# Performance work log

Hardware: AMD Instinct MI355X
Metric: run time of the kernel (lower is better)

Reference implementation:

```python
import jax, jax.numpy as jnp
import numpy as np

N, E, D, R = 50000, 800000, 64, 65


def setup_inputs() -> dict:
    key = jax.random.key(0)
    ks = jax.random.split(key, 8)
    x = jax.random.normal(ks[0], (N, D), dtype=jnp.float32)
    src = jax.random.randint(ks[1], (E,), 0, N, dtype=jnp.int32)
    dst = jax.random.randint(ks[2], (E,), 0, N, dtype=jnp.int32)
    edge_type = jax.random.randint(ks[3], (E,), 0, R, dtype=jnp.int32)
    s = 1.0 / np.sqrt(D)
    W1 = jax.random.normal(ks[4], (R, D, D), dtype=jnp.float32) * s
    Wl1 = jax.random.normal(ks[5], (D, D), dtype=jnp.float32) * s
    W2 = jax.random.normal(ks[6], (R, D, D), dtype=jnp.float32) * s
    Wl2 = jax.random.normal(ks[7], (D, D), dtype=jnp.float32) * s
    return {"x": x, "src": src, "dst": dst, "edge_type": edge_type,
            "W1": W1, "Wl1": Wl1, "W2": W2, "Wl2": Wl2}


def _rgcn_layer(x, src, dst, edge_type, W, Wl):
    # x: [N, D_in], W: [R, D_in, D_out], Wl: [D_in, D_out]
    n = x.shape[0]
    r = W.shape[0]
    # per-relation transform of all node features: [R, N, D_out]
    xw = jnp.einsum('nd,rdh->rnh', x, W)
    # gather transformed source feature for each edge by its relation: [E, D_out]
    msg = xw[edge_type, src]
    # mean aggregation per (destination node, relation) as in PyG RGCNConv
    key = dst.astype(jnp.int32) * r + edge_type
    cnt = jax.ops.segment_sum(jnp.ones(key.shape, x.dtype), key, num_segments=n * r)
    norm = 1.0 / jnp.maximum(cnt[key], 1.0)  # [E]
    agg = jax.ops.segment_sum(msg * norm[:, None], dst, num_segments=n)  # [N, D_out]
    # self-loop linear term (self_loop_weights in original module)
    out = agg + x @ Wl
    # activation; dropout is identity in eval mode; batch norm disabled
    return jax.nn.relu(out)


def reference(x, src, dst, edge_type, W1, Wl1, W2, Wl2):
    h = _rgcn_layer(x, src, dst, edge_type, W1, Wl1)
    h = _rgcn_layer(h, src, dst, edge_type, W2, Wl2)
    return h
```

## Files before the change

kernel.cpp:

```cpp
#include <hip/hip_runtime.h>

typedef __attribute__((ext_vector_type(8))) short bf16x8;
typedef __attribute__((ext_vector_type(4))) float f32x4;
typedef __attribute__((ext_vector_type(2))) unsigned int u32x2;

constexpr int D = 64;
constexpr int SEG = 64;
constexpr int CSTR = 16;

__device__ inline unsigned short f2bf(float f) {
  unsigned u = __float_as_uint(f);
  u += 0x7fff + ((u >> 16) & 1);
  return (unsigned short)(u >> 16);
}
__device__ inline float bflo(unsigned u) { return __uint_as_float(u << 16); }
__device__ inline float bfhi(unsigned u) { return __uint_as_float(u & 0xffff0000u); }

__global__ __launch_bounds__(256) void count_kernel(
    const int* __restrict__ dst, const int* __restrict__ et,
    int* __restrict__ bcnt, int* __restrict__ deg, int E, int R, int nbE) {
  __shared__ int lh[128];
  int t = threadIdx.x;
  if (t < 128) lh[t] = 0;
  __syncthreads();
  int e = blockIdx.x * 256 + t;
  if (e < E) {
    atomicAdd(&deg[(long)dst[e] * CSTR], 1);
    atomicAdd(&lh[et[e]], 1);
  }
  __syncthreads();
  if (t < R) bcnt[t * nbE + blockIdx.x] = lh[t];
}

__global__ __launch_bounds__(256) void scanA_dual_kernel(
    const int* __restrict__ bcnt, const int* __restrict__ deg,
    int* __restrict__ bsum, int nBC, int N, int nbBC) {
  __shared__ int s[256];
  int t = threadIdx.x;
  int b = blockIdx.x;
  int v;
  if (b < nbBC) {
    int i = b * 256 + t;
    v = (i < nBC) ? bcnt[i] : 0;
  } else {
    int i = (b - nbBC) * 256 + t;
    v = (i < N) ? deg[(long)i * CSTR] : 0;
  }
  s[t] = v;
  __syncthreads();
  for (int o = 128; o > 0; o >>= 1) {
    if (t < o) s[t] += s[t + o];
    __syncthreads();
  }
  if (t == 0) bsum[b] = s[0];
}

__device__ inline void scanB_region(int* bsum, int nb, int t) {
  __shared__ int s[256];
  __shared__ int carry;
  if (t == 0) carry = 0;
  __syncthreads();
  for (int base = 0; base < nb; base += 256) {
    int i = base + t;
    int v = (i < nb) ? bsum[i] : 0;
    s[t] = v;
    __syncthreads();
    for (int o = 1; o < 256; o <<= 1) {
      int u = (t >= o) ? s[t - o] : 0;
      __syncthreads();
      s[t] += u;
      __syncthreads();
    }
    if (i < nb) bsum[i] = carry + s[t] - v;
    __syncthreads();
    if (t == 0) carry += s[255];
    __syncthreads();
  }
}

__global__ __launch_bounds__(256) void scanB_dual_kernel(
    int* __restrict__ bsum, int nbBC, int nbN) {
  int t = threadIdx.x;
  scanB_region(bsum, nbBC, t);
  scanB_region(bsum + nbBC, nbN, t);
}

__global__ __launch_bounds__(256) void scanC_dual_kernel(
    const int* __restrict__ bcnt, const int* __restrict__ deg,
    const int* __restrict__ bsum, int* __restrict__ prefE,
    int* __restrict__ dstoff, int* __restrict__ cur2,
    int nBC, int N, int nbBC) {
  __shared__ int s[256];
  int t = threadIdx.x;
  int b = blockIdx.x;
  bool isBC = (b < nbBC);
  int i = (isBC ? b : b - nbBC) * 256 + t;
  int n = isBC ? nBC : N;
  int v = 0;
  if (i < n) v = isBC ? bcnt[i] : deg[(long)i * CSTR];
  s[t] = v;
  __syncthreads();
  for (int o = 1; o < 256; o <<= 1) {
    int u = (t >= o) ? s[t - o] : 0;
    __syncthreads();
    s[t] += u;
    __syncthreads();
  }
  int excl = bsum[b] + s[t] - v;
  if (isBC) {
    if (i < n) prefE[i] = excl;
    if (i == n - 1) prefE[n] = excl + v;
  } else {
    if (i < n) { dstoff[i] = excl; cur2[(long)i * CSTR] = excl; }
    if (i == n - 1) dstoff[n] = excl + v;
  }
}

__global__ void prefix_wrel_kernel(const int* __restrict__ prefE,
                                   int* __restrict__ cursor, int* __restrict__ wrel,
                                   int nbE, int R) {
  __shared__ int sc[128];
  int l = threadIdx.x;
  int c = 0;
  if (l < R) {
    int tot = prefE[(l + 1) * nbE] - prefE[l * nbE];
    c = (tot + SEG - 1) & ~(SEG - 1);
  }
  sc[l] = c;
  __syncthreads();
  for (int ofs = 1; ofs < 128; ofs <<= 1) {
    int v = (l >= ofs) ? sc[l - ofs] : 0;
    __syncthreads();
    sc[l] += v;
    __syncthreads();
  }
  if (l < R) {
    int cur = sc[l] - c;
    cursor[l] = cur;
    int w0 = cur >> 6;
    int nw = c >> 6;
    for (int w = 0; w < nw; ++w) wrel[w0 + w] = l;
  }
}

__global__ __launch_bounds__(256) void scatter_kernel(
    const int* __restrict__ src, const int* __restrict__ dst, const int* __restrict__ et,
    const int* __restrict__ cursor, const int* __restrict__ prefE,
    int* __restrict__ cur2, int2* __restrict__ eidx,
    int E, int R, int nbE) {
  __shared__ int lh[128];
  __shared__ int lbase[128];
  int t = threadIdx.x, b = blockIdx.x;
  if (t < R) {
    lh[t] = 0;
    lbase[t] = cursor[t] + prefE[t * nbE + b] - prefE[t * nbE];
  }
  __syncthreads();
  int e = b * 256 + t;
  if (e < E) {
    int r = et[e], s = src[e], d = dst[e];
    int lr = atomicAdd(&lh[r], 1);
    int jd = atomicAdd(&cur2[(long)d * CSTR], 1);
    int pos = lbase[r] + lr;
    eidx[pos] = make_int2(s, jd);
  }
}

__global__ __launch_bounds__(256) void cvt_all_kernel(
    const float* __restrict__ x, unsigned short* __restrict__ xb, int nx,
    const float* __restrict__ W1, unsigned short* __restrict__ WT1,
    const float* __restrict__ W2, unsigned short* __restrict__ WT2, int nw,
    const float* __restrict__ Wl1, unsigned short* __restrict__ WTl1,
    const float* __restrict__ Wl2, unsigned short* __restrict__ WTl2, int nl) {
  int i = blockIdx.x * 256 + threadIdx.x;
  if (i < nx) { xb[i] = f2bf(x[i]); return; }
  i -= nx;
  if (i < 2 * nw) {
    const float* W = (i < nw) ? W1 : W2;
    unsigned short* WT = (i < nw) ? WT1 : WT2;
    int i2 = (i < nw) ? i : i - nw;
    int n = i2 & 63, k = (i2 >> 6) & 63, r = i2 >> 12;
    WT[(r << 12) + (n << 6) + k] = f2bf(W[(r << 12) + (k << 6) + n]);
    return;
  }
  i -= 2 * nw;
  if (i < 2 * nl) {
    const float* W = (i < nl) ? Wl1 : Wl2;
    unsigned short* WT = (i < nl) ? WTl1 : WTl2;
    int i2 = (i < nl) ? i : i - nl;
    int n = i2 & 63, k = (i2 >> 6) & 63;
    WT[(n << 6) + k] = f2bf(W[(k << 6) + n]);
  }
}

__global__ __launch_bounds__(256)
void msg_kernel(const unsigned short* __restrict__ xb,
                const unsigned short* __restrict__ WT,
                const int2* __restrict__ eidx, const int* __restrict__ wrel,
                unsigned int* __restrict__ msgp, int* __restrict__ relrow, int nwaves) {
  const int lane = (int)threadIdx.x & 63;
  const int l15 = lane & 15;
  const int q = lane >> 4;
  const int wave = blockIdx.x * 4 + ((int)threadIdx.x >> 6);
  if (wave >= nwaves) return;
  const long base = (long)wave * SEG;
  const int r = wrel[wave];
  const unsigned short* wb = WT + ((long)r << 12);
  bf16x8 Bf[4][2];
#pragma unroll
  for (int nt = 0; nt < 4; ++nt)
#pragma unroll
    for (int kh = 0; kh < 2; ++kh)
      Bf[nt][kh] = *(const bf16x8*)(wb + (nt * 16 + l15) * 64 + kh * 32 + q * 8);
#pragma unroll
  for (int t = 0; t < 4; ++t) {
    int2 rec = eidx[base + t * 16 + l15];
    if (relrow && lane < 16 && rec.y >= 0) relrow[rec.y] = r;
    const unsigned short* xr = xb + ((long)max(rec.x, 0) << 6);
    bf16x8 A0 = *(const bf16x8*)(xr + q * 8);
    bf16x8 A1 = *(const bf16x8*)(xr + 32 + q * 8);
    f32x4 acc0 = (f32x4)0.0f, acc1 = (f32x4)0.0f, acc2 = (f32x4)0.0f, acc3 = (f32x4)0.0f;
    acc0 = __builtin_amdgcn_mfma_f32_16x16x32_bf16(A0, Bf[0][0], acc0, 0, 0, 0);
    acc0 = __builtin_amdgcn_mfma_f32_16x16x32_bf16(A1, Bf[0][1], acc0, 0, 0, 0);
    acc1 = __builtin_amdgcn_mfma_f32_16x16x32_bf16(A0, Bf[1][0], acc1, 0, 0, 0);
    acc1 = __builtin_amdgcn_mfma_f32_16x16x32_bf16(A1, Bf[1][1], acc1, 0, 0, 0);
    acc2 = __builtin_amdgcn_mfma_f32_16x16x32_bf16(A0, Bf[2][0], acc2, 0, 0, 0);
    acc2 = __builtin_amdgcn_mfma_f32_16x16x32_bf16(A1, Bf[2][1], acc2, 0, 0, 0);
    acc3 = __builtin_amdgcn_mfma_f32_16x16x32_bf16(A0, Bf[3][0], acc3, 0, 0, 0);
    acc3 = __builtin_amdgcn_mfma_f32_16x16x32_bf16(A1, Bf[3][1], acc3, 0, 0, 0);
#pragma unroll
    for (int rg = 0; rg < 4; ++rg) {
      int row = q * 4 + rg;
      int jd = __shfl(rec.y, row);
      if (jd >= 0) {
        unsigned p0 = (unsigned)f2bf(acc0[rg]) | ((unsigned)f2bf(acc1[rg]) << 16);
        unsigned p1 = (unsigned)f2bf(acc2[rg]) | ((unsigned)f2bf(acc3[rg]) << 16);
        u32x2 pk;
        pk.x = p0; pk.y = p1;
        *(u32x2*)(msgp + (long)jd * 32 + 2 * l15) = pk;
      }
    }
  }
}

__global__ __launch_bounds__(256) void weight_kernel(
    const int* __restrict__ relrow, const int* __restrict__ dstoff,
    float* __restrict__ wrow, int N) {
  __shared__ int rsh[4][256];
  const int wv = (int)threadIdx.x >> 6;
  const int lane = (int)threadIdx.x & 63;
  const int d = blockIdx.x * 4 + wv;
  if (d >= N) return;
  const int off = dstoff[d], end = dstoff[d + 1];
  const int deg = end - off;
  if (deg <= 0) return;
  if (deg <= 256) {
    const int nit = (deg + 63) >> 6;
    for (int it = 0; it < nit; ++it) {
      int l = it * 64 + lane;
      if (l < deg) rsh[wv][l] = relrow[off + l];
    }
    __threadfence_block();
    for (int it = 0; it < nit; ++it) {
      int l = it * 64 + lane;
      if (l < deg) {
        int rv = rsh[wv][l];
        int c = 0;
        for (int m = 0; m < deg; ++m) c += (rsh[wv][m] == rv) ? 1 : 0;
        wrow[off + l] = 1.0f / (float)c;
      }
    }
  } else {
    for (int l = lane; l < deg; l += 64) {
      int rv = relrow[off + l];
      int c = 0;
      for (int m = off; m < end; ++m) c += (relrow[m] == rv) ? 1 : 0;
      wrow[off + l] = 1.0f / (float)c;
    }
  }
}

__global__ __launch_bounds__(256) void agg_kernel(
    const unsigned int* __restrict__ msgp, const int* __restrict__ dstoff,
    const float* __restrict__ wrow, float* __restrict__ agg, int N) {
  const int lane = (int)threadIdx.x & 63;
  const int j = lane & 31;
  const int half = lane >> 5;
  const int d = blockIdx.x * 4 + ((int)threadIdx.x >> 6);
  if (d >= N) return;
  const int off = dstoff[d], end = dstoff[d + 1];
  float a0 = 0.f, a1 = 0.f, b0 = 0.f, b1 = 0.f;
  float c0 = 0.f, c1 = 0.f, e0 = 0.f, e1 = 0.f;
  int i = off + half;
  for (; i + 6 < end; i += 8) {
    float w0 = wrow[i];
    float w1 = wrow[i + 2];
    float w2 = wrow[i + 4];
    float w3 = wrow[i + 6];
    unsigned u0 = msgp[(long)i * 32 + j];
    unsigned u1 = msgp[(long)(i + 2) * 32 + j];
    unsigned u2 = msgp[(long)(i + 4) * 32 + j];
    unsigned u3 = msgp[(long)(i + 6) * 32 + j];
    a0 = fmaf(w0, bflo(u0), a0);
    a1 = fmaf(w0, bfhi(u0), a1);
    b0 = fmaf(w1, bflo(u1), b0);
    b1 = fmaf(w1, bfhi(u1), b1);
    c0 = fmaf(w2, bflo(u2), c0);
    c1 = fmaf(w2, bfhi(u2), c1);
    e0 = fmaf(w3, bflo(u3), e0);
    e1 = fmaf(w3, bfhi(u3), e1);
  }
  for (; i + 2 < end; i += 4) {
    float w0 = wrow[i];
    float w1 = wrow[i + 2];
    unsigned u0 = msgp[(long)i * 32 + j];
    unsigned u1 = msgp[(long)(i + 2) * 32 + j];
    a0 = fmaf(w0, bflo(u0), a0);
    a1 = fmaf(w0, bfhi(u0), a1);
    b0 = fmaf(w1, bflo(u1), b0);
    b1 = fmaf(w1, bfhi(u1), b1);
  }
  if (i < end) {
    float w0 = wrow[i];
    unsigned u0 = msgp[(long)i * 32 + j];
    a0 = fmaf(w0, bflo(u0), a0);
    a1 = fmaf(w0, bfhi(u0), a1);
  }
  float aLo = (a0 + b0) + (c0 + e0), aHi = (a1 + b1) + (c1 + e1);
  aLo += __shfl_xor(aLo, 32);
  aHi += __shfl_xor(aHi, 32);
  if (half == 0) {
    const int k = j >> 1;
    int colLo = (j & 1) ? 32 + k : k;
    agg[(long)d * D + colLo] = aLo;
    agg[(long)d * D + colLo + 16] = aHi;
  }
}

__global__ __launch_bounds__(256) void selfloop_kernel(
    const unsigned short* __restrict__ xbin, const unsigned short* __restrict__ WTl,
    const float* __restrict__ agg, float* __restrict__ outp,
    unsigned short* __restrict__ hb, int N) {
  const int lane = (int)threadIdx.x & 63;
  const int l15 = lane & 15;
  const int q = lane >> 4;
  const int wave = blockIdx.x * 4 + ((int)threadIdx.x >> 6);
  const int base = wave * 64;
  if (base >= N) return;
  bf16x8 Bf[4][2];
#pragma unroll
  for (int nt = 0; nt < 4; ++nt)
#pragma unroll
    for (int kh = 0; kh < 2; ++kh)
      Bf[nt][kh] = *(const bf16x8*)(WTl + (nt * 16 + l15) * 64 + kh * 32 + q * 8);
#pragma unroll
  for (int t = 0; t < 4; ++t) {
    const int row0 = base + t * 16;
    if (row0 >= N) break;
    const int m = min(row0 + l15, N - 1);
    const unsigned short* xr = xbin + ((long)m << 6);
    bf16x8 A0 = *(const bf16x8*)(xr + q * 8);
    bf16x8 A1 = *(const bf16x8*)(xr + 32 + q * 8);
    f32x4 acc[4];
#pragma unroll
    for (int nt = 0; nt < 4; ++nt) {
#pragma unroll
      for (int rg = 0; rg < 4; ++rg) {
        int node = row0 + q * 4 + rg;
        acc[nt][rg] = (node < N) ? agg[(long)node * D + nt * 16 + l15] : 0.0f;
      }
    }
#pragma unroll
    for (int nt = 0; nt < 4; ++nt) {
      acc[nt] = __builtin_amdgcn_mfma_f32_16x16x32_bf16(A0, Bf[nt][0], acc[nt], 0, 0, 0);
      acc[nt] = __builtin_amdgcn_mfma_f32_16x16x32_bf16(A1, Bf[nt][1], acc[nt], 0, 0, 0);
    }
#pragma unroll
    for (int rg = 0; rg < 4; ++rg) {
      int node = row0 + q * 4 + rg;
      if (node < N) {
#pragma unroll
        for (int nt = 0; nt < 4; ++nt) {
          float v = fmaxf(acc[nt][rg], 0.0f);
          if (outp) outp[(long)node * D + nt * 16 + l15] = v;
          if (hb) hb[(long)node * D + nt * 16 + l15] = f2bf(v);
        }
      }
    }
  }
}

extern "C" void kernel_launch(void* const* d_in, const int* in_sizes, int n_in,
                              void* d_out, int out_size, void* d_ws, size_t ws_size,
                              hipStream_t stream) {
  const float* x   = (const float*)d_in[0];
  const int* src   = (const int*)d_in[1];
  const int* dst   = (const int*)d_in[2];
  const int* et    = (const int*)d_in[3];
  const float* W1  = (const float*)d_in[4];
  const float* Wl1 = (const float*)d_in[5];
  const float* W2  = (const float*)d_in[6];
  const float* Wl2 = (const float*)d_in[7];
  float* out = (float*)d_out;

  const int N = in_sizes[0] / D;
  const int E = in_sizes[1];
  const int R = in_sizes[4] / (D * D);

  const int Ecap = ((E + SEG - 1) & ~(SEG - 1)) + R * SEG;
  const int nwaves = Ecap / SEG;
  const int nbN = (N + 255) / 256;
  const int nbE = (E + 255) / 256;
  const int nBC = R * nbE;
  const int nbBC = (nBC + 255) / 256;

  char* ws = (char*)d_ws;
  size_t off = 0;
  auto alloc = [&](size_t bytes) -> void* {
    void* p = (void*)(ws + off);
    off += (bytes + 255) & ~(size_t)255;
    return p;
  };
  int*   cursor = (int*)alloc((size_t)R * sizeof(int));
  int*   deg    = (int*)alloc((size_t)N * CSTR * sizeof(int));
  int*   cur2   = (int*)alloc((size_t)N * CSTR * sizeof(int));
  int*   bcnt   = (int*)alloc((size_t)nBC * sizeof(int));
  int*   prefE  = (int*)alloc((size_t)(nBC + 1) * sizeof(int));
  int*   bsum   = (int*)alloc((size_t)(nbBC + nbN) * sizeof(int));
  int*   dstoff = (int*)alloc((size_t)(N + 1) * sizeof(int));
  int*   relrow = (int*)alloc((size_t)E * sizeof(int));
  float* wrow   = (float*)alloc((size_t)E * sizeof(float));
  int*   wrel   = (int*)alloc((size_t)nwaves * sizeof(int));
  int2*  eidx   = (int2*)alloc((size_t)(Ecap + SEG) * sizeof(int2));
  unsigned int* msgp = (unsigned int*)alloc((size_t)E * 32 * sizeof(unsigned int));
  float* agg    = (float*)alloc((size_t)N * D * sizeof(float));
  unsigned short* xb  = (unsigned short*)alloc((size_t)N * D * sizeof(unsigned short));
  unsigned short* hb  = (unsigned short*)alloc((size_t)N * D * sizeof(unsigned short));
  unsigned short* WT1 = (unsigned short*)alloc((size_t)R * D * D * sizeof(unsigned short));
  unsigned short* WT2 = (unsigned short*)alloc((size_t)R * D * D * sizeof(unsigned short));
  unsigned short* WTl1 = (unsigned short*)alloc((size_t)D * D * sizeof(unsigned short));
  unsigned short* WTl2 = (unsigned short*)alloc((size_t)D * D * sizeof(unsigned short));
  (void)ws_size; (void)n_in; (void)out_size;

  const int msg_blocks = (nwaves + 3) / 4;
  const int agg_blocks = (N + 3) / 4;
  const int sl_blocks = ((N + 63) / 64 + 3) / 4;
  const int nx = N * D;
  const int nw = R * D * D;
  const int nl = D * D;
  const int cvt_total = nx + 2 * nw + 2 * nl;

  hipMemsetAsync(deg, 0, (size_t)N * CSTR * sizeof(int), stream);
  hipMemsetAsync(wrel, 0, (size_t)nwaves * sizeof(int), stream);
  hipMemsetAsync(eidx, 0xFF, (size_t)(Ecap + SEG) * sizeof(int2), stream);
  count_kernel<<<nbE, 256, 0, stream>>>(dst, et, bcnt, deg, E, R, nbE);
  scanA_dual_kernel<<<nbBC + nbN, 256, 0, stream>>>(bcnt, deg, bsum, nBC, N, nbBC);
  scanB_dual_kernel<<<1, 256, 0, stream>>>(bsum, nbBC, nbN);
  scanC_dual_kernel<<<nbBC + nbN, 256, 0, stream>>>(bcnt, deg, bsum, prefE,
                                                    dstoff, cur2, nBC, N, nbBC);
  prefix_wrel_kernel<<<1, 128, 0, stream>>>(prefE, cursor, wrel, nbE, R);
  scatter_kernel<<<nbE, 256, 0, stream>>>(src, dst, et, cursor, prefE, cur2,
                                          eidx, E, R, nbE);
  cvt_all_kernel<<<(cvt_total + 255) / 256, 256, 0, stream>>>(
      x, xb, nx, W1, WT1, W2, WT2, nw, Wl1, WTl1, Wl2, WTl2, nl);

  msg_kernel<<<msg_blocks, 256, 0, stream>>>(xb, WT1, eidx, wrel, msgp, relrow, nwaves);
  weight_kernel<<<agg_blocks, 256, 0, stream>>>(relrow, dstoff, wrow, N);
  agg_kernel<<<agg_blocks, 256, 0, stream>>>(msgp, dstoff, wrow, agg, N);
  selfloop_kernel<<<sl_blocks, 256, 0, stream>>>(xb, WTl1, agg, nullptr, hb, N);

  msg_kernel<<<msg_blocks, 256, 0, stream>>>(hb, WT2, eidx, wrel, msgp, nullptr, nwaves);
  agg_kernel<<<agg_blocks, 256, 0, stream>>>(msgp, dstoff, wrow, agg, N);
  selfloop_kernel<<<sl_blocks, 256, 0, stream>>>(hb, WTl2, agg, out, nullptr, N);
}
```

Measured before the change: 337.0 us.

## Fuse aggregation with self-loop GEMM, move relrow to scatter, drop memsets, swizzle blocks

Merges the aggregation and self-loop kernels so each 64-node block keeps its aggregated rows in shared memory, removing the fp32 agg buffer round trip through global memory. Writes relrow during scatter so the weight kernel can run before layer 1 messaging. The two memsets are replaced by padding writes inside the prefix kernel. msg_kernel also gets an XCD-aware block index swizzle for L2 locality. Each aggsl block now handles 16 nodes per wave serially, which lowers parallelism for the aggregation phase.

```diff
diff --git a/kernel.cpp b/kernel.cpp
--- a/kernel.cpp
+++ b/kernel.cpp
@@ -118,12 +118,13 @@
 
 __global__ void prefix_wrel_kernel(const int* __restrict__ prefE,
                                    int* __restrict__ cursor, int* __restrict__ wrel,
-                                   int nbE, int R) {
+                                   int2* __restrict__ eidx,
+                                   int nbE, int R, int Ecap, int nwavesTot) {
   __shared__ int sc[128];
   int l = threadIdx.x;
-  int c = 0;
+  int tot = 0, c = 0;
   if (l < R) {
-    int tot = prefE[(l + 1) * nbE] - prefE[l * nbE];
+    tot = prefE[(l + 1) * nbE] - prefE[l * nbE];
     c = (tot + SEG - 1) & ~(SEG - 1);
   }
   sc[l] = c;
@@ -140,13 +141,17 @@
     int w0 = cur >> 6;
     int nw = c >> 6;
     for (int w = 0; w < nw; ++w) wrel[w0 + w] = l;
-  }
+    for (int p = cur + tot; p < cur + c; ++p) eidx[p] = make_int2(-1, -1);
+  }
+  int total = sc[127];
+  for (int p = total + l; p < Ecap; p += 128) eidx[p] = make_int2(-1, -1);
+  for (int w = (total >> 6) + l; w < nwavesTot; w += 128) wrel[w] = 0;
 }
 
 __global__ __launch_bounds__(256) void scatter_kernel(
     const int* __restrict__ src, const int* __restrict__ dst, const int* __restrict__ et,
     const int* __restrict__ cursor, const int* __restrict__ prefE,
-    int* __restrict__ cur2, int2* __restrict__ eidx,
+    int* __restrict__ cur2, int2* __restrict__ eidx, int* __restrict__ relrow,
     int E, int R, int nbE) {
   __shared__ int lh[128];
   __shared__ int lbase[128];
@@ -163,6 +168,7 @@
     int jd = atomicAdd(&cur2[(long)d * CSTR], 1);
     int pos = lbase[r] + lr;
     eidx[pos] = make_int2(s, jd);
+    relrow[jd] = r;
   }
 }
 
@@ -197,11 +203,16 @@
 void msg_kernel(const unsigned short* __restrict__ xb,
                 const unsigned short* __restrict__ WT,
                 const int2* __restrict__ eidx, const int* __restrict__ wrel,
-                unsigned int* __restrict__ msgp, int* __restrict__ relrow, int nwaves) {
+                unsigned int* __restrict__ msgp, int nwaves) {
   const int lane = (int)threadIdx.x & 63;
   const int l15 = lane & 15;
   const int q = lane >> 4;
-  const int wave = blockIdx.x * 4 + ((int)threadIdx.x >> 6);
+  const int nwg = (int)gridDim.x;
+  const int bid = (int)blockIdx.x;
+  const int xcd = bid & 7, idx = bid >> 3;
+  const int qq = nwg >> 3, rr = nwg & 7;
+  const int swz = (xcd < rr ? xcd * (qq + 1) : rr * (qq + 1) + (xcd - rr) * qq) + idx;
+  const int wave = swz * 4 + ((int)threadIdx.x >> 6);
   if (wave >= nwaves) return;
   const long base = (long)wave * SEG;
   const int r = wrel[wave];
@@ -215,7 +226,6 @@
 #pragma unroll
   for (int t = 0; t < 4; ++t) {
     int2 rec = eidx[base + t * 16 + l15];
-    if (relrow && lane < 16 && rec.y >= 0) relrow[rec.y] = r;
     const unsigned short* xr = xb + ((long)max(rec.x, 0) << 6);
     bf16x8 A0 = *(const bf16x8*)(xr + q * 8);
     bf16x8 A1 = *(const bf16x8*)(xr + 32 + q * 8);
@@ -280,111 +290,105 @@
   }
 }
 
-__global__ __launch_bounds__(256) void agg_kernel(
+__global__ __launch_bounds__(256) void aggsl_kernel(
     const unsigned int* __restrict__ msgp, const int* __restrict__ dstoff,
-    const float* __restrict__ wrow, float* __restrict__ agg, int N) {
+    const float* __restrict__ wrow,
+    const unsigned short* __restrict__ xbin, const unsigned short* __restrict__ WTl,
+    float* __restrict__ outp, unsigned short* __restrict__ hb, int N) {
+  __shared__ float aggs[64][66];
   const int lane = (int)threadIdx.x & 63;
+  const int wv = (int)threadIdx.x >> 6;
+  const int base = blockIdx.x * 64;
   const int j = lane & 31;
   const int half = lane >> 5;
-  const int d = blockIdx.x * 4 + ((int)threadIdx.x >> 6);
-  if (d >= N) return;
-  const int off = dstoff[d], end = dstoff[d + 1];
-  float a0 = 0.f, a1 = 0.f, b0 = 0.f, b1 = 0.f;
-  float c0 = 0.f, c1 = 0.f, e0 = 0.f, e1 = 0.f;
-  int i = off + half;
-  for (; i + 6 < end; i += 8) {
-    float w0 = wrow[i];
-    float w1 = wrow[i + 2];
-    float w2 = wrow[i + 4];
-    float w3 = wrow[i + 6];
-    unsigned u0 = msgp[(long)i * 32 + j];
-    unsigned u1 = msgp[(long)(i + 2) * 32 + j];
-    unsigned u2 = msgp[(long)(i + 4) * 32 + j];
-    unsigned u3 = msgp[(long)(i + 6) * 32 + j];
-    a0 = fmaf(w0, bflo(u0), a0);
-    a1 = fmaf(w0, bfhi(u0), a1);
-    b0 = fmaf(w1, bflo(u1), b0);
-    b1 = fmaf(w1, bfhi(u1), b1);
-    c0 = fmaf(w2, bflo(u2), c0);
-    c1 = fmaf(w2, bfhi(u2), c1);
-    e0 = fmaf(w3, bflo(u3), e0);
-    e1 = fmaf(w3, bfhi(u3), e1);
-  }
-  for (; i + 2 < end; i += 4) {
-    float w0 = wrow[i];
-    float w1 = wrow[i + 2];
-    unsigned u0 = msgp[(long)i * 32 + j];
-    unsigned u1 = msgp[(long)(i + 2) * 32 + j];
-    a0 = fmaf(w0, bflo(u0), a0);
-    a1 = fmaf(w0, bfhi(u0), a1);
-    b0 = fmaf(w1, bflo(u1), b0);
-    b1 = fmaf(w1, bfhi(u1), b1);
-  }
-  if (i < end) {
-    float w0 = wrow[i];
-    unsigned u0 = msgp[(long)i * 32 + j];
-    a0 = fmaf(w0, bflo(u0), a0);
-    a1 = fmaf(w0, bfhi(u0), a1);
-  }
-  float aLo = (a0 + b0) + (c0 + e0), aHi = (a1 + b1) + (c1 + e1);
-  aLo += __shfl_xor(aLo, 32);
-  aHi += __shfl_xor(aHi, 32);
-  if (half == 0) {
-    const int k = j >> 1;
-    int colLo = (j & 1) ? 32 + k : k;
-    agg[(long)d * D + colLo] = aLo;
-    agg[(long)d * D + colLo + 16] = aHi;
-  }
-}
-
-__global__ __launch_bounds__(256) void selfloop_kernel(
-    const unsigned short* __restrict__ xbin, const unsigned short* __restrict__ WTl,
-    const float* __restrict__ agg, float* __restrict__ outp,
-    unsigned short* __restrict__ hb, int N) {
-  const int lane = (int)threadIdx.x & 63;
+  for (int i16 = 0; i16 < 16; ++i16) {
+    const int d = base + wv * 16 + i16;
+    if (d >= N) break;
+    const int off = dstoff[d], end = dstoff[d + 1];
+    float a0 = 0.f, a1 = 0.f, b0 = 0.f, b1 = 0.f;
+    float c0 = 0.f, c1 = 0.f, e0 = 0.f, e1 = 0.f;
+    int i = off + half;
+    for (; i + 6 < end; i += 8) {
+      float w0 = wrow[i];
+      float w1 = wrow[i + 2];
+      float w2 = wrow[i + 4];
+      float w3 = wrow[i + 6];
+      unsigned u0 = msgp[(long)i * 32 + j];
+      unsigned u1 = msgp[(long)(i + 2) * 32 + j];
+      unsigned u2 = msgp[(long)(i + 4) * 32 + j];
+      unsigned u3 = msgp[(long)(i + 6) * 32 + j];
+      a0 = fmaf(w0, bflo(u0), a0);
+      a1 = fmaf(w0, bfhi(u0), a1);
+      b0 = fmaf(w1, bflo(u1), b0);
+      b1 = fmaf(w1, bfhi(u1), b1);
+      c0 = fmaf(w2, bflo(u2), c0);
+      c1 = fmaf(w2, bfhi(u2), c1);
+      e0 = fmaf(w3, bflo(u3), e0);
+      e1 = fmaf(w3, bfhi(u3), e1);
+    }
+    for (; i + 2 < end; i += 4) {
+      float w0 = wrow[i];
+      float w1 = wrow[i + 2];
+      unsigned u0 = msgp[(long)i * 32 + j];
+      unsigned u1 = msgp[(long)(i + 2) * 32 + j];
+      a0 = fmaf(w0, bflo(u0), a0);
+      a1 = fmaf(w0, bfhi(u0), a1);
+      b0 = fmaf(w1, bflo(u1), b0);
+      b1 = fmaf(w1, bfhi(u1), b1);
+    }
+    if (i < end) {
+      float w0 = wrow[i];
+      unsigned u0 = msgp[(long)i * 32 + j];
+      a0 = fmaf(w0, bflo(u0), a0);
+      a1 = fmaf(w0, bfhi(u0), a1);
+    }
+    float aLo = (a0 + b0) + (c0 + e0), aHi = (a1 + b1) + (c1 + e1);
+    aLo += __shfl_xor(aLo, 32);
+    aHi += __shfl_xor(aHi, 32);
+    if (half == 0) {
+      const int k = j >> 1;
+      const int colLo = (j & 1) ? 32 + k : k;
+      aggs[d - base][colLo] = aLo;
+      aggs[d - base][colLo + 16] = aHi;
+    }
+  }
+  __syncthreads();
   const int l15 = lane & 15;
   const int q = lane >> 4;
-  const int wave = blockIdx.x * 4 + ((int)threadIdx.x >> 6);
-  const int base = wave * 64;
-  if (base >= N) return;
+  const int row0 = base + wv * 16;
+  if (row0 >= N) return;
   bf16x8 Bf[4][2];
 #pragma unroll
   for (int nt = 0; nt < 4; ++nt)
 #pragma unroll
     for (int kh = 0; kh < 2; ++kh)
       Bf[nt][kh] = *(const bf16x8*)(WTl + (nt * 16 + l15) * 64 + kh * 32 + q * 8);
-#pragma unroll
-  for (int t = 0; t < 4; ++t) {
-    const int row0 = base + t * 16;
-    if (row0 >= N) break;
-    const int m = min(row0 + l15, N - 1);
-    const unsigned short* xr = xbin + ((long)m << 6);
-    bf16x8 A0 = *(const bf16x8*)(xr + q * 8);
-    bf16x8 A1 = *(const bf16x8*)(xr + 32 + q * 8);
-    f32x4 acc[4];
-#pragma unroll
-    for (int nt = 0; nt < 4; ++nt) {
-#pragma unroll
-      for (int rg = 0; rg < 4; ++rg) {
-        int node = row0 + q * 4 + rg;
-        acc[nt][rg] = (node < N) ? agg[(long)node * D + nt * 16 + l15] : 0.0f;
-      }
-    }
-#pragma unroll
-    for (int nt = 0; nt < 4; ++nt) {
-      acc[nt] = __builtin_amdgcn_mfma_f32_16x16x32_bf16(A0, Bf[nt][0], acc[nt], 0, 0, 0);
-      acc[nt] = __builtin_amdgcn_mfma_f32_16x16x32_bf16(A1, Bf[nt][1], acc[nt], 0, 0, 0);
-    }
+  const int m = min(row0 + l15, N - 1);
+  const unsigned short* xr = xbin + ((long)m << 6);
+  bf16x8 A0 = *(const bf16x8*)(xr + q * 8);
+  bf16x8 A1 = *(const bf16x8*)(xr + 32 + q * 8);
+  f32x4 acc[4];
+#pragma unroll
+  for (int nt = 0; nt < 4; ++nt)
 #pragma unroll
     for (int rg = 0; rg < 4; ++rg) {
       int node = row0 + q * 4 + rg;
-      if (node < N) {
-#pragma unroll
-        for (int nt = 0; nt < 4; ++nt) {
-          float v = fmaxf(acc[nt][rg], 0.0f);
-          if (outp) outp[(long)node * D + nt * 16 + l15] = v;
-          if (hb) hb[(long)node * D + nt * 16 + l15] = f2bf(v);
-        }
+      acc[nt][rg] = (node < N) ? aggs[wv * 16 + q * 4 + rg][nt * 16 + l15] : 0.0f;
+    }
+#pragma unroll
+  for (int nt = 0; nt < 4; ++nt) {
+    acc[nt] = __builtin_amdgcn_mfma_f32_16x16x32_bf16(A0, Bf[nt][0], acc[nt], 0, 0, 0);
+    acc[nt] = __builtin_amdgcn_mfma_f32_16x16x32_bf16(A1, Bf[nt][1], acc[nt], 0, 0, 0);
+  }
+#pragma unroll
+  for (int rg = 0; rg < 4; ++rg) {
+    int node = row0 + q * 4 + rg;
+    if (node < N) {
+#pragma unroll
+      for (int nt = 0; nt < 4; ++nt) {
+        float v = fmaxf(acc[nt][rg], 0.0f);
+        if (outp) outp[(long)node * D + nt * 16 + l15] = v;
+        if (hb) hb[(long)node * D + nt * 16 + l15] = f2bf(v);
       }
     }
   }
@@ -433,7 +437,6 @@
   int*   wrel   = (int*)alloc((size_t)nwaves * sizeof(int));
   int2*  eidx   = (int2*)alloc((size_t)(Ecap + SEG) * sizeof(int2));
   unsigned int* msgp = (unsigned int*)alloc((size_t)E * 32 * sizeof(unsigned int));
-  float* agg    = (float*)alloc((size_t)N * D * sizeof(float));
   unsigned short* xb  = (unsigned short*)alloc((size_t)N * D * sizeof(unsigned short));
   unsigned short* hb  = (unsigned short*)alloc((size_t)N * D * sizeof(unsigned short));
   unsigned short* WT1 = (unsigned short*)alloc((size_t)R * D * D * sizeof(unsigned short));
@@ -443,33 +446,32 @@
   (void)ws_size; (void)n_in; (void)out_size;
 
   const int msg_blocks = (nwaves + 3) / 4;
-  const int agg_blocks = (N + 3) / 4;
-  const int sl_blocks = ((N + 63) / 64 + 3) / 4;
+  const int w_blocks = (N + 3) / 4;
+  const int aggsl_blocks = (N + 63) / 64;
   const int nx = N * D;
   const int nw = R * D * D;
   const int nl = D * D;
   const int cvt_total = nx + 2 * nw + 2 * nl;
 
   hipMemsetAsync(deg, 0, (size_t)N * CSTR * sizeof(int), stream);
-  hipMemsetAsync(wrel, 0, (size_t)nwaves * sizeof(int), stream);
-  hipMemsetAsync(eidx, 0xFF, (size_t)(Ecap + SEG) * sizeof(int2), stream);
   count_kernel<<<nbE, 256, 0, stream>>>(dst, et, bcnt, deg, E, R, nbE);
   scanA_dual_kernel<<<nbBC + nbN, 256, 0, stream>>>(bcnt, deg, bsum, nBC, N, nbBC);
   scanB_dual_kernel<<<1, 256, 0, stream>>>(bsum, nbBC, nbN);
   scanC_dual_kernel<<<nbBC + nbN, 256, 0, stream>>>(bcnt, deg, bsum, prefE,
                                                     dstoff, cur2, nBC, N, nbBC);
-  prefix_wrel_kernel<<<1, 128, 0, stream>>>(prefE, cursor, wrel, nbE, R);
+  prefix_wrel_kernel<<<1, 128, 0, stream>>>(prefE, cursor, wrel, eidx,
+                                            nbE, R, Ecap, nwaves);
   scatter_kernel<<<nbE, 256, 0, stream>>>(src, dst, et, cursor, prefE, cur2,
-                                          eidx, E, R, nbE);
+                                          eidx, relrow, E, R, nbE);
+  weight_kernel<<<w_blocks, 256, 0, stream>>>(relrow, dstoff, wrow, N);
   cvt_all_kernel<<<(cvt_total + 255) / 256, 256, 0, stream>>>(
       x, xb, nx, W1, WT1, W2, WT2, nw, Wl1, WTl1, Wl2, WTl2, nl);
 
-  msg_kernel<<<msg_blocks, 256, 0, stream>>>(xb, WT1, eidx, wrel, msgp, relrow, nwaves);
-  weight_kernel<<<agg_blocks, 256, 0, stream>>>(relrow, dstoff, wrow, N);
-  agg_kernel<<<agg_blocks, 256, 0, stream>>>(msgp, dstoff, wrow, agg, N);
-  selfloop_kernel<<<sl_blocks, 256, 0, stream>>>(xb, WTl1, agg, nullptr, hb, N);
-
-  msg_kernel<<<msg_blocks, 256, 0, stream>>>(hb, WT2, eidx, wrel, msgp, nullptr, nwaves);
-  agg_kernel<<<agg_blocks, 256, 0, stream>>>(msgp, dstoff, wrow, agg, N);
-  selfloop_kernel<<<sl_blocks, 256, 0, stream>>>(hb, WTl2, agg, out, nullptr, N);
-}
+  msg_kernel<<<msg_blocks, 256, 0, stream>>>(xb, WT1, eidx, wrel, msgp, nwaves);
+  aggsl_kernel<<<aggsl_blocks, 256, 0, stream>>>(msgp, dstoff, wrow, xb, WTl1,
+                                                 nullptr, hb, N);
+
+  msg_kernel<<<msg_blocks, 256, 0, stream>>>(hb, WT2, eidx, wrel, msgp, nwaves);
+  aggsl_kernel<<<aggsl_blocks, 256, 0, stream>>>(msgp, dstoff, wrow, hb, WTl2,
+                                                 out, nullptr, N);
+}
```

Result: no change. 343.1 us (+1.8%).
